# Performance work log

Hardware: AMD Instinct MI355X
Metric: run time of the kernel (lower is better)

## Reference

```python
import jax, jax.numpy as jnp
import numpy as np

B, T, H = 1024, 256, 128

def _gru(x, Wx, Wh, b):
    # Keras GRU (reset_after=True), gate order z, r, h. x: [B,T,D], b: [2,3H]
    xp = x @ Wx + b[0]                      # [B,T,3H]
    h0 = jnp.zeros((x.shape[0], Wh.shape[0]), x.dtype)
    def step(h, xt):
        hp = h @ Wh + b[1]
        xz, xr, xh = jnp.split(xt, 3, axis=-1)
        hz, hr, hn = jnp.split(hp, 3, axis=-1)
        z = jax.nn.sigmoid(xz + hz)
        r = jax.nn.sigmoid(xr + hr)
        hh = jnp.tanh(xh + r * hn)
        return z * h + (1.0 - z) * hh, None
    h, _ = jax.lax.scan(step, h0, jnp.swapaxes(xp, 0, 1))
    return h                                 # [B,H]

def setup_inputs() -> dict:
    key = jax.random.key(0)
    ks = jax.random.split(key, 32)
    def gp(k, shape, scale=0.05):
        return (jax.random.normal(k, shape, dtype=jnp.float32) * scale)
    inp = {
        "spatial": jax.random.normal(ks[0], (B, T, 2), dtype=jnp.float32),
        "hour_idx": jax.random.randint(ks[1], (B, T), 0, 24, dtype=jnp.int32),
        "week_idx": jax.random.randint(ks[2], (B, T), 0, 7, dtype=jnp.int32),
        "E_time": gp(ks[3], (24, H)),
        "E_week": gp(ks[4], (7, H)),
        # spatial GRU (input dim 2)
        "Ws_x": gp(ks[5], (2, 3 * H)), "Ws_h": gp(ks[6], (H, 3 * H)), "bs": gp(ks[7], (2, 3 * H)),
        # hour temporal GRU (input dim 128)
        "Wh_x": gp(ks[8], (H, 3 * H)), "Wh_h": gp(ks[9], (H, 3 * H)), "bh": gp(ks[10], (2, 3 * H)),
        # week temporal GRU (input dim 128)
        "Ww_x": gp(ks[11], (H, 3 * H)), "Ww_h": gp(ks[12], (H, 3 * H)), "bw": gp(ks[13], (2, 3 * H)),
        # attention Dense(3) over the channel axis of size 3
        "Wa": gp(ks[14], (3, 3)), "ba": gp(ks[15], (3,)),
        # MLP
        "W1": gp(ks[16], (H, 1024)), "b1": gp(ks[17], (1024,)),
        "W2": gp(ks[18], (1024, 512)), "b2": gp(ks[19], (512,)),
        "W3": gp(ks[20], (512, 256)), "b3": gp(ks[21], (256,)),
        "W4": gp(ks[22], (256, H)), "b4": gp(ks[23], (H,)),
        "Wo": gp(ks[24], (H, 1)), "bo": gp(ks[25], (1,)),
    }
    return inp

def reference(spatial, hour_idx, week_idx, E_time, E_week,
              Ws_x, Ws_h, bs, Wh_x, Wh_h, bh, Ww_x, Ww_h, bw,
              Wa, ba, W1, b1, W2, b2, W3, b3, W4, b4, Wo, bo):
    te = E_time[hour_idx]                    # [B,T,128] gather
    we = E_week[week_idx]                    # [B,T,128] gather
    fs = _gru(spatial, Ws_x, Ws_h, bs)       # [B,128]
    fh = _gru(te, Wh_x, Wh_h, bh)            # [B,128]
    fw = _gru(we, Ww_x, Ww_h, bw)            # [B,128]
    allf = jnp.stack([fs, fh, fw], axis=-1)  # [B,128,3]
    scores = jax.nn.softmax(jax.nn.relu(allf @ Wa + ba), axis=-1)
    sf = jnp.sum(allf * scores, axis=-1)     # [B,128] attention-fused features
    x = jax.nn.relu(sf @ W1 + b1)
    x = jax.nn.relu(x @ W2 + b2)
    x = jax.nn.relu(x @ W3 + b3)
    x = jax.nn.relu(x @ W4 + b4)
    out = (x + sf) @ Wo + bo                 # residual then Dense(1)
    return out[:, 0]                         # [B]
```

## Files before the change

### kernel.cpp

```cpp
#include <hip/hip_runtime.h>
#include <hip/hip_bf16.h>

typedef __attribute__((ext_vector_type(8))) short short8;
typedef __attribute__((ext_vector_type(4))) float f32x4;
typedef __attribute__((ext_vector_type(2))) float f32x2;

#define LOG2E  1.44269504088896340736f
#define NLOG2E (-1.44269504088896340736f)
#define TLOG2E (2.88539008177792681472f)

#define HES 168

__device__ __forceinline__ unsigned short f2bf(float f) {
  unsigned u = __builtin_bit_cast(unsigned, f);
  u += 0x7fffu + ((u >> 16) & 1u);
  return (unsigned short)(u >> 16);
}

__global__ void setup_kernel(
    const float* __restrict__ E_time, const float* __restrict__ E_week,
    const float* __restrict__ Wh_x, const float* __restrict__ bh,
    const float* __restrict__ Ww_x, const float* __restrict__ bw,
    const float* __restrict__ W1, const float* __restrict__ W2,
    const float* __restrict__ W3, const float* __restrict__ W4,
    float* __restrict__ Ptime, float* __restrict__ Pweek,
    unsigned short* __restrict__ Wt)
{
  const int b = blockIdx.x;
  const int tid = threadIdx.x;
  if (b < 31) {
    const int c = tid;
    if (b < 24) {
      float acc = bh[c];
      for (int d = 0; d < 128; ++d)
        acc = fmaf(E_time[b * 128 + d], Wh_x[d * 384 + c], acc);
      Ptime[b * 384 + c] = acc;
    } else {
      const int r = b - 24;
      float acc = bw[c];
      for (int d = 0; d < 128; ++d)
        acc = fmaf(E_week[r * 128 + d], Ww_x[d * 384 + c], acc);
      Pweek[r * 384 + c] = acc;
    }
    return;
  }
  const int id = (b - 31) * 384 + tid;
  if (id >= 819200) return;
  if (id < 131072) {
    const int n = id >> 7, k = id & 127;
    Wt[id] = f2bf(W1[k * 1024 + n]);
  } else if (id < 655360) {
    const int off = id - 131072, n = off >> 10, k = off & 1023;
    Wt[id] = f2bf(W2[k * 512 + n]);
  } else if (id < 786432) {
    const int off = id - 655360, n = off >> 9, k = off & 511;
    Wt[id] = f2bf(W3[k * 256 + n]);
  } else {
    const int off = id - 786432, n = off >> 8, k = off & 255;
    Wt[id] = f2bf(W4[k * 128 + n]);
  }
}

__global__ __launch_bounds__(512, 2) void gru_kernel(
    const float* __restrict__ spatial,
    const int* __restrict__ hour_idx,
    const int* __restrict__ week_idx,
    const float* __restrict__ Ws_x,
    const float* __restrict__ Ws_h, const float* __restrict__ bs,
    const float* __restrict__ Wh_h, const float* __restrict__ bh,
    const float* __restrict__ Ww_h, const float* __restrict__ bw,
    const float* __restrict__ Ptime, const float* __restrict__ Pweek,
    float* __restrict__ fs, float* __restrict__ fh, float* __restrict__ fw)
{
  __shared__ __align__(16) unsigned short hx[2][16 * HES];

  const int tid  = threadIdx.x;
  const int lane = tid & 63;
  const int wv   = tid >> 6;
  const int ar   = lane & 15;
  const int akg  = lane >> 4;
  const int gid  = blockIdx.x;
  const int gru  = gid >> 6;
  const int row0 = (gid & 63) * 16;

  const float* __restrict__ Wh   = (gru == 0) ? Ws_h : (gru == 1) ? Wh_h : Ww_h;
  const float* __restrict__ bvec = (gru == 0) ? bs   : (gru == 1) ? bh   : bw;
  float* __restrict__ fout       = (gru == 0) ? fs   : (gru == 1) ? fh   : fw;
  const float* __restrict__ Ptab = (gru == 1) ? Ptime : Pweek;
  const int* __restrict__ idxg   = (gru == 1) ? hour_idx : week_idx;
  const int NR = (gru == 1) ? 24 : 7;

  const int j = wv * 16 + ar;

  short8 wf[15];
  #pragma unroll
  for (int g = 0; g < 2; ++g) {
    #pragma unroll
    for (int ks = 0; ks < 5; ++ks) {
      short8 f;
      #pragma unroll
      for (int q = 0; q < 8; ++q) {
        const int k = ks * 32 + akg * 8 + q;
        float v;
        if (k < 128) v = Wh[k * 384 + g * 128 + j];
        else {
          const int p = k - 128;
          if (gru == 0) v = (p == 0) ? Ws_x[g * 128 + j]
                          : (p == 1) ? Ws_x[384 + g * 128 + j] : 0.f;
          else          v = (p < NR) ? Ptab[p * 384 + g * 128 + j] : 0.f;
        }
        f[q] = (short)f2bf(v * NLOG2E);
      }
      wf[g * 5 + ks] = f;
    }
  }
  #pragma unroll
  for (int ks = 0; ks < 4; ++ks) {
    short8 f;
    #pragma unroll
    for (int q = 0; q < 8; ++q) {
      const int k = ks * 32 + akg * 8 + q;
      f[q] = (short)f2bf(Wh[k * 384 + 256 + j] * TLOG2E);
    }
    wf[10 + ks] = f;
  }
  {
    short8 f;
    #pragma unroll
    for (int q = 0; q < 8; ++q) {
      const int p = akg * 8 + q;
      float v;
      if (gru == 0) v = (p == 0) ? Ws_x[256 + j]
                      : (p == 1) ? Ws_x[384 + 256 + j] : 0.f;
      else          v = (p < NR) ? Ptab[p * 384 + 256 + j] : 0.f;
      f[q] = (short)f2bf(v * TLOG2E);
    }
    wf[14] = f;
  }

  const float bz  = (bvec[384 + j]       + (gru == 0 ? bvec[j]       : 0.f)) * NLOG2E;
  const float br  = (bvec[384 + 128 + j] + (gru == 0 ? bvec[128 + j] : 0.f)) * NLOG2E;
  const float bnh = bvec[384 + 256 + j] * TLOG2E;
  const float bnx = (gru == 0 ? bvec[256 + j] : 0.f) * TLOG2E;

  for (int e = tid; e < 2 * 16 * HES; e += 512) ((unsigned short*)hx)[e] = 0;
  __syncthreads();

  const bool mt  = (tid & 31) == 0;
  const int mrow = tid >> 5;
  int ix_prev = 0, ix_cur = 0;
  if (mt) {
    if (gru == 0) {
      const f32x2 s = *(const f32x2*)&spatial[(row0 + mrow) * 512];
      unsigned pk;
      asm("v_cvt_pk_bf16_f32 %0, %1, %2" : "=v"(pk) : "v"(s.x), "v"(s.y));
      *(unsigned*)&hx[0][mrow * HES + 128] = pk;
    } else {
      ix_cur = idxg[(row0 + mrow) * 256];
      hx[0][mrow * HES + 128 + ix_cur] = 0x3F80;
    }
  }
  __syncthreads();

  float hst[4] = {0.f, 0.f, 0.f, 0.f};

  for (int t = 0; t < 256; ++t) {
    const unsigned short* __restrict__ hb = hx[t & 1];
    unsigned short* __restrict__ ho       = hx[(t + 1) & 1];

    short8 a[5];
    #pragma unroll
    for (int ks = 0; ks < 5; ++ks)
      a[ks] = *(const short8*)&hb[ar * HES + ks * 32 + akg * 8];

    f32x2 msp = {0.f, 0.f};
    int ix_next = 0;
    const bool mact = mt && (t + 1 < 256);
    if (mact) {
      if (gru == 0) msp = *(const f32x2*)&spatial[(row0 + mrow) * 512 + 2 * (t + 1)];
      else          ix_next = idxg[(row0 + mrow) * 256 + t + 1];
    }

    f32x4 az  = {bz, bz, bz, bz};
    f32x4 arr = {br, br, br, br};
    f32x4 anh = {bnh, bnh, bnh, bnh};
    f32x4 anx = {bnx, bnx, bnx, bnx};
    #pragma unroll
    for (int ks = 0; ks < 4; ++ks) {
      az  = __builtin_amdgcn_mfma_f32_16x16x32_bf16(a[ks], wf[ks],      az,  0, 0, 0);
      arr = __builtin_amdgcn_mfma_f32_16x16x32_bf16(a[ks], wf[5 + ks],  arr, 0, 0, 0);
      anh = __builtin_amdgcn_mfma_f32_16x16x32_bf16(a[ks], wf[10 + ks], anh, 0, 0, 0);
    }
    az  = __builtin_amdgcn_mfma_f32_16x16x32_bf16(a[4], wf[4],  az,  0, 0, 0);
    arr = __builtin_amdgcn_mfma_f32_16x16x32_bf16(a[4], wf[9],  arr, 0, 0, 0);
    anx = __builtin_amdgcn_mfma_f32_16x16x32_bf16(a[4], wf[14], anx, 0, 0, 0);

    if (mact) {
      if (gru == 0) {
        unsigned pk;
        asm("v_cvt_pk_bf16_f32 %0, %1, %2" : "=v"(pk) : "v"(msp.x), "v"(msp.y));
        *(unsigned*)&ho[mrow * HES + 128] = pk;
      } else {
        if (t >= 1) ho[mrow * HES + 128 + ix_prev] = 0;
        ho[mrow * HES + 128 + ix_next] = 0x3F80;
        ix_prev = ix_cur; ix_cur = ix_next;
      }
    }

    float hn4[4];
    #pragma unroll
    for (int q = 0; q < 4; ++q) {
      const float z  = __builtin_amdgcn_rcpf(1.f + __builtin_amdgcn_exp2f(az[q]));
      const float r  = __builtin_amdgcn_rcpf(1.f + __builtin_amdgcn_exp2f(arr[q]));
      const float e  = __builtin_amdgcn_exp2f(fmaf(r, anh[q], anx[q]));
      const float hh = fmaf(-2.f, __builtin_amdgcn_rcpf(e + 1.f), 1.f);
      hn4[q] = fmaf(z, hst[q] - hh, hh);
      hst[q] = hn4[q];
    }

    #pragma unroll
    for (int q = 0; q < 4; ++q)
      ho[(akg * 4 + q) * HES + j] = f2bf(hn4[q]);

    __syncthreads();
  }

  #pragma unroll
  for (int q = 0; q < 4; ++q)
    fout[(row0 + akg * 4 + q) * 128 + j] = hst[q];
}

template<int K, int N>
__device__ __forceinline__ void mlp_layer(
    const unsigned short* __restrict__ xin, unsigned short* __restrict__ xout,
    const unsigned short* __restrict__ Wt, const float* __restrict__ bias,
    int lane, int wv, float* __restrict__ foutF)
{
  constexpr int NT = N / 64;
  const int ar  = lane & 15;
  const int akg = lane >> 4;
  f32x4 acc[NT];
  #pragma unroll
  for (int nt = 0; nt < NT; ++nt) acc[nt] = f32x4{0.f, 0.f, 0.f, 0.f};
  for (int ks = 0; ks < K / 32; ++ks) {
    const short8 a = *(const short8*)&xin[ar * 1032 + ks * 32 + akg * 8];
    #pragma unroll
    for (int nt = 0; nt < NT; ++nt) {
      const int n = wv * (N / 4) + nt * 16 + ar;
      const short8 b = *(const short8*)&Wt[n * K + ks * 32 + akg * 8];
      acc[nt] = __builtin_amdgcn_mfma_f32_16x16x32_bf16(a, b, acc[nt], 0, 0, 0);
    }
  }
  const int rbase = akg * 4;
  #pragma unroll
  for (int nt = 0; nt < NT; ++nt) {
    const int n = wv * (N / 4) + nt * 16 + ar;
    const float bv = bias[n];
    #pragma unroll
    for (int q = 0; q < 4; ++q) {
      float v = acc[nt][q] + bv;
      v = fmaxf(v, 0.f);
      xout[(rbase + q) * 1032 + n] = f2bf(v);
      if (foutF) foutF[(rbase + q) * 128 + n] = v;
    }
  }
}

__global__ __launch_bounds__(256) void attn_mlp_kernel(
    const float* __restrict__ fs, const float* __restrict__ fh, const float* __restrict__ fw,
    const float* __restrict__ Wa, const float* __restrict__ ba,
    const unsigned short* __restrict__ Wt,
    const float* __restrict__ b1, const float* __restrict__ b2,
    const float* __restrict__ b3, const float* __restrict__ b4,
    const float* __restrict__ Wo, const float* __restrict__ bo,
    float* __restrict__ out)
{
  __shared__ __align__(16) unsigned short xa[16 * 1032];
  __shared__ __align__(16) unsigned short xb[16 * 1032];
  __shared__ __align__(16) float sf_l[16 * 128];
  __shared__ __align__(16) float x4f[16 * 128];

  const int tid  = threadIdx.x;
  const int lane = tid & 63;
  const int wv   = tid >> 6;
  const int row0 = blockIdx.x * 16;

  {
    const int i  = tid >> 4;
    const int j0 = (tid & 15) * 8;
    float wa[9], bav[3];
    #pragma unroll
    for (int q = 0; q < 9; ++q) wa[q] = Wa[q];
    #pragma unroll
    for (int q = 0; q < 3; ++q) bav[q] = ba[q];
    const int base = (row0 + i) * 128 + j0;
    #pragma unroll
    for (int half = 0; half < 2; ++half) {
      const f32x4 a = *(const f32x4*)&fs[base + half * 4];
      const f32x4 b = *(const f32x4*)&fh[base + half * 4];
      const f32x4 c = *(const f32x4*)&fw[base + half * 4];
      #pragma unroll
      for (int q = 0; q < 4; ++q) {
        const float f0 = a[q], f1 = b[q], f2 = c[q];
        float s0 = f0 * wa[0] + f1 * wa[3] + f2 * wa[6] + bav[0];
        float s1 = f0 * wa[1] + f1 * wa[4] + f2 * wa[7] + bav[1];
        float s2 = f0 * wa[2] + f1 * wa[5] + f2 * wa[8] + bav[2];
        s0 = fmaxf(s0, 0.f); s1 = fmaxf(s1, 0.f); s2 = fmaxf(s2, 0.f);
        const float m  = fmaxf(s0, fmaxf(s1, s2));
        const float e0 = __builtin_amdgcn_exp2f((s0 - m) * LOG2E);
        const float e1 = __builtin_amdgcn_exp2f((s1 - m) * LOG2E);
        const float e2 = __builtin_amdgcn_exp2f((s2 - m) * LOG2E);
        const float inv = __builtin_amdgcn_rcpf(e0 + e1 + e2);
        const float sf  = (f0 * e0 + f1 * e1 + f2 * e2) * inv;
        const int jj = j0 + half * 4 + q;
        sf_l[i * 128 + jj] = sf;
        xa[i * 1032 + jj]  = f2bf(sf);
      }
    }
  }
  __syncthreads();

  mlp_layer<128, 1024>(xa, xb, Wt,          b1, lane, wv, nullptr);
  __syncthreads();
  mlp_layer<1024, 512>(xb, xa, Wt + 131072, b2, lane, wv, nullptr);
  __syncthreads();
  mlp_layer<512,  256>(xa, xb, Wt + 655360, b3, lane, wv, nullptr);
  __syncthreads();
  mlp_layer<256,  128>(xb, xa, Wt + 786432, b4, lane, wv, x4f);
  __syncthreads();

  const int row = tid >> 4;
  const int p   = tid & 15;
  float part = 0.f;
  #pragma unroll
  for (int q = 0; q < 8; ++q) {
    const int jj = p + q * 16;
    part += (x4f[row * 128 + jj] + sf_l[row * 128 + jj]) * Wo[jj];
  }
  #pragma unroll
  for (int off = 8; off > 0; off >>= 1)
    part += __shfl_xor(part, off, 16);
  if (p == 0) out[row0 + row] = part + bo[0];
}

extern "C" void kernel_launch(void* const* d_in, const int* in_sizes, int n_in,
                              void* d_out, int out_size, void* d_ws, size_t ws_size,
                              hipStream_t stream) {
  const float* spatial  = (const float*)d_in[0];
  const int*   hour_idx = (const int*)d_in[1];
  const int*   week_idx = (const int*)d_in[2];
  const float* E_time   = (const float*)d_in[3];
  const float* E_week   = (const float*)d_in[4];
  const float* Ws_x = (const float*)d_in[5];
  const float* Ws_h = (const float*)d_in[6];
  const float* bs   = (const float*)d_in[7];
  const float* Wh_x = (const float*)d_in[8];
  const float* Wh_h = (const float*)d_in[9];
  const float* bh   = (const float*)d_in[10];
  const float* Ww_x = (const float*)d_in[11];
  const float* Ww_h = (const float*)d_in[12];
  const float* bw   = (const float*)d_in[13];
  const float* Wa   = (const float*)d_in[14];
  const float* ba   = (const float*)d_in[15];
  const float* W1   = (const float*)d_in[16];
  const float* b1   = (const float*)d_in[17];
  const float* W2   = (const float*)d_in[18];
  const float* b2   = (const float*)d_in[19];
  const float* W3   = (const float*)d_in[20];
  const float* b3   = (const float*)d_in[21];
  const float* W4   = (const float*)d_in[22];
  const float* b4   = (const float*)d_in[23];
  const float* Wo   = (const float*)d_in[24];
  const float* bo   = (const float*)d_in[25];
  float* out = (float*)d_out;

  float* ws    = (float*)d_ws;
  float* Ptime = ws;
  float* Pweek = Ptime + 9216;
  float* fsb   = Pweek + 2688;
  float* fhb   = fsb + 131072;
  float* fwb   = fhb + 131072;
  unsigned short* Wt = (unsigned short*)(fwb + 131072);

  setup_kernel<<<31 + 2134, 384, 0, stream>>>(E_time, E_week, Wh_x, bh, Ww_x, bw,
      W1, W2, W3, W4, Ptime, Pweek, Wt);
  gru_kernel<<<192, 512, 0, stream>>>(spatial, hour_idx, week_idx, Ws_x,
      Ws_h, bs, Wh_h, bh, Ww_h, bw, Ptime, Pweek, fsb, fhb, fwb);
  attn_mlp_kernel<<<64, 256, 0, stream>>>(fsb, fhb, fwb, Wa, ba, Wt,
      b1, b2, b3, b4, Wo, bo, out);
}
```

Measured before the change: 240.7 us.

## Stagger GRU row halves to overlap gate math with MFMAs; tile weight transpose

The GRU recurrence now uses a single hidden-state buffer and splits each wave's rows into two groups advancing half a step apart. While one group's gate nonlinearities and state writes run, the MFMAs for the other group's next step are issued, aiming to hide the latency of the serial gate chain. The cost is twice as many MFMA passes and barriers per timestep, since each pass computes all 16 rows but only half are consumed. Separately, the bf16 weight transpose in the setup kernel now goes through a 64x64 shared-memory tile, so both the global reads and the global writes are coalesced.

```diff
diff --git a/kernel.cpp b/kernel.cpp
--- a/kernel.cpp
+++ b/kernel.cpp
@@ -17,7 +17,7 @@
   return (unsigned short)(u >> 16);
 }
 
-__global__ void setup_kernel(
+__global__ __launch_bounds__(256) void setup_kernel(
     const float* __restrict__ E_time, const float* __restrict__ E_week,
     const float* __restrict__ Wh_x, const float* __restrict__ bh,
     const float* __restrict__ Ww_x, const float* __restrict__ bw,
@@ -29,36 +29,38 @@
   const int b = blockIdx.x;
   const int tid = threadIdx.x;
   if (b < 31) {
-    const int c = tid;
-    if (b < 24) {
-      float acc = bh[c];
-      for (int d = 0; d < 128; ++d)
-        acc = fmaf(E_time[b * 128 + d], Wh_x[d * 384 + c], acc);
-      Ptime[b * 384 + c] = acc;
-    } else {
-      const int r = b - 24;
-      float acc = bw[c];
-      for (int d = 0; d < 128; ++d)
-        acc = fmaf(E_week[r * 128 + d], Ww_x[d * 384 + c], acc);
-      Pweek[r * 384 + c] = acc;
+    for (int c = tid; c < 384; c += 256) {
+      if (b < 24) {
+        float acc = bh[c];
+        for (int d = 0; d < 128; ++d)
+          acc = fmaf(E_time[b * 128 + d], Wh_x[d * 384 + c], acc);
+        Ptime[b * 384 + c] = acc;
+      } else {
+        const int r = b - 24;
+        float acc = bw[c];
+        for (int d = 0; d < 128; ++d)
+          acc = fmaf(E_week[r * 128 + d], Ww_x[d * 384 + c], acc);
+        Pweek[r * 384 + c] = acc;
+      }
     }
     return;
   }
-  const int id = (b - 31) * 384 + tid;
-  if (id >= 819200) return;
-  if (id < 131072) {
-    const int n = id >> 7, k = id & 127;
-    Wt[id] = f2bf(W1[k * 1024 + n]);
-  } else if (id < 655360) {
-    const int off = id - 131072, n = off >> 10, k = off & 1023;
-    Wt[id] = f2bf(W2[k * 512 + n]);
-  } else if (id < 786432) {
-    const int off = id - 655360, n = off >> 9, k = off & 511;
-    Wt[id] = f2bf(W3[k * 256 + n]);
-  } else {
-    const int off = id - 786432, n = off >> 8, k = off & 255;
-    Wt[id] = f2bf(W4[k * 128 + n]);
-  }
+  __shared__ float tile[64][65];
+  int tb = b - 31;
+  const float* src; unsigned short* dst; int K, N, tk, tn;
+  if (tb < 32)       { src = W1; dst = Wt;          K = 128;  N = 1024; tk = tb >> 4; tn = tb & 15; }
+  else if (tb < 160) { tb -= 32;  src = W2; dst = Wt + 131072; K = 1024; N = 512;  tk = tb >> 3; tn = tb & 7; }
+  else if (tb < 192) { tb -= 160; src = W3; dst = Wt + 655360; K = 512;  N = 256;  tk = tb >> 2; tn = tb & 3; }
+  else               { tb -= 192; src = W4; dst = Wt + 786432; K = 256;  N = 128;  tk = tb >> 1; tn = tb & 1; }
+  const int tx = tid & 63, ty = tid >> 6;
+  const int k0 = tk * 64, n0 = tn * 64;
+  #pragma unroll
+  for (int i = 0; i < 16; ++i)
+    tile[ty * 16 + i][tx] = src[(k0 + ty * 16 + i) * N + n0 + tx];
+  __syncthreads();
+  #pragma unroll
+  for (int i = 0; i < 16; ++i)
+    dst[(n0 + ty * 16 + i) * K + k0 + tx] = f2bf(tile[tx][ty * 16 + i]);
 }
 
 __global__ __launch_bounds__(512, 2) void gru_kernel(
@@ -72,7 +74,7 @@
     const float* __restrict__ Ptime, const float* __restrict__ Pweek,
     float* __restrict__ fs, float* __restrict__ fh, float* __restrict__ fw)
 {
-  __shared__ __align__(16) unsigned short hx[2][16 * HES];
+  __shared__ __align__(16) unsigned short hx[16 * HES];
 
   const int tid  = threadIdx.x;
   const int lane = tid & 63;
@@ -143,91 +145,111 @@
   const float bnh = bvec[384 + 256 + j] * TLOG2E;
   const float bnx = (gru == 0 ? bvec[256 + j] : 0.f) * TLOG2E;
 
-  for (int e = tid; e < 2 * 16 * HES; e += 512) ((unsigned short*)hx)[e] = 0;
-  __syncthreads();
-
-  const bool mt  = (tid & 31) == 0;
-  const int mrow = tid >> 5;
-  int ix_prev = 0, ix_cur = 0;
+  for (int e = tid; e < 16 * HES; e += 512) hx[e] = 0;
+  __syncthreads();
+
+  const bool mt   = (tid & 31) == 0;
+  const int mrow  = tid >> 5;
+  const int mgrp  = (mrow >> 1) & 1;
+  f32x2 spn = {0.f, 0.f};
+  int ixc = 0, ixn = 0;
   if (mt) {
     if (gru == 0) {
-      const f32x2 s = *(const f32x2*)&spatial[(row0 + mrow) * 512];
+      const f32x2 s0 = *(const f32x2*)&spatial[(row0 + mrow) * 512];
       unsigned pk;
-      asm("v_cvt_pk_bf16_f32 %0, %1, %2" : "=v"(pk) : "v"(s.x), "v"(s.y));
-      *(unsigned*)&hx[0][mrow * HES + 128] = pk;
+      asm("v_cvt_pk_bf16_f32 %0, %1, %2" : "=v"(pk) : "v"(s0.x), "v"(s0.y));
+      *(unsigned*)&hx[mrow * HES + 128] = pk;
+      spn = *(const f32x2*)&spatial[(row0 + mrow) * 512 + 2];
     } else {
-      ix_cur = idxg[(row0 + mrow) * 256];
-      hx[0][mrow * HES + 128 + ix_cur] = 0x3F80;
+      ixc = idxg[(row0 + mrow) * 256];
+      hx[mrow * HES + 128 + ixc] = 0x3F80;
+      ixn = idxg[(row0 + mrow) * 256 + 1];
     }
   }
   __syncthreads();
 
   float hst[4] = {0.f, 0.f, 0.f, 0.f};
-
-  for (int t = 0; t < 256; ++t) {
-    const unsigned short* __restrict__ hb = hx[t & 1];
-    unsigned short* __restrict__ ho       = hx[(t + 1) & 1];
-
-    short8 a[5];
-    #pragma unroll
-    for (int ks = 0; ks < 5; ++ks)
-      a[ks] = *(const short8*)&hb[ar * HES + ks * 32 + akg * 8];
-
-    f32x2 msp = {0.f, 0.f};
-    int ix_next = 0;
-    const bool mact = mt && (t + 1 < 256);
-    if (mact) {
-      if (gru == 0) msp = *(const f32x2*)&spatial[(row0 + mrow) * 512 + 2 * (t + 1)];
-      else          ix_next = idxg[(row0 + mrow) * 256 + t + 1];
-    }
-
-    f32x4 az  = {bz, bz, bz, bz};
-    f32x4 arr = {br, br, br, br};
-    f32x4 anh = {bnh, bnh, bnh, bnh};
-    f32x4 anx = {bnx, bnx, bnx, bnx};
-    #pragma unroll
-    for (int ks = 0; ks < 4; ++ks) {
-      az  = __builtin_amdgcn_mfma_f32_16x16x32_bf16(a[ks], wf[ks],      az,  0, 0, 0);
-      arr = __builtin_amdgcn_mfma_f32_16x16x32_bf16(a[ks], wf[5 + ks],  arr, 0, 0, 0);
-      anh = __builtin_amdgcn_mfma_f32_16x16x32_bf16(a[ks], wf[10 + ks], anh, 0, 0, 0);
-    }
-    az  = __builtin_amdgcn_mfma_f32_16x16x32_bf16(a[4], wf[4],  az,  0, 0, 0);
-    arr = __builtin_amdgcn_mfma_f32_16x16x32_bf16(a[4], wf[9],  arr, 0, 0, 0);
-    anx = __builtin_amdgcn_mfma_f32_16x16x32_bf16(a[4], wf[14], anx, 0, 0, 0);
-
-    if (mact) {
-      if (gru == 0) {
-        unsigned pk;
-        asm("v_cvt_pk_bf16_f32 %0, %1, %2" : "=v"(pk) : "v"(msp.x), "v"(msp.y));
-        *(unsigned*)&ho[mrow * HES + 128] = pk;
-      } else {
-        if (t >= 1) ho[mrow * HES + 128 + ix_prev] = 0;
-        ho[mrow * HES + 128 + ix_next] = 0x3F80;
-        ix_prev = ix_cur; ix_cur = ix_next;
-      }
-    }
-
-    float hn4[4];
-    #pragma unroll
-    for (int q = 0; q < 4; ++q) {
-      const float z  = __builtin_amdgcn_rcpf(1.f + __builtin_amdgcn_exp2f(az[q]));
-      const float r  = __builtin_amdgcn_rcpf(1.f + __builtin_amdgcn_exp2f(arr[q]));
-      const float e  = __builtin_amdgcn_exp2f(fmaf(r, anh[q], anx[q]));
-      const float hh = fmaf(-2.f, __builtin_amdgcn_rcpf(e + 1.f), 1.f);
-      hn4[q] = fmaf(z, hst[q] - hh, hh);
-      hst[q] = hn4[q];
-    }
-
-    #pragma unroll
-    for (int q = 0; q < 4; ++q)
-      ho[(akg * 4 + q) * HES + j] = f2bf(hn4[q]);
-
+  const int abase = ar * HES;
+
+#define DSREAD(AV) { _Pragma("unroll") \
+  for (int ks = 0; ks < 5; ++ks) \
+    AV[ks] = *(const short8*)&hx[abase + ks * 32 + akg * 8]; }
+
+#define MFMA_ALL(AV, AZ, AR_, ANH, ANX) { \
+  AZ  = (f32x4){bz, bz, bz, bz}; \
+  AR_ = (f32x4){br, br, br, br}; \
+  ANH = (f32x4){bnh, bnh, bnh, bnh}; \
+  ANX = (f32x4){bnx, bnx, bnx, bnx}; \
+  _Pragma("unroll") for (int ks = 0; ks < 4; ++ks) { \
+    AZ  = __builtin_amdgcn_mfma_f32_16x16x32_bf16(AV[ks], wf[ks],      AZ,  0, 0, 0); \
+    AR_ = __builtin_amdgcn_mfma_f32_16x16x32_bf16(AV[ks], wf[5 + ks],  AR_, 0, 0, 0); \
+    ANH = __builtin_amdgcn_mfma_f32_16x16x32_bf16(AV[ks], wf[10 + ks], ANH, 0, 0, 0); } \
+  AZ  = __builtin_amdgcn_mfma_f32_16x16x32_bf16(AV[4], wf[4],  AZ,  0, 0, 0); \
+  AR_ = __builtin_amdgcn_mfma_f32_16x16x32_bf16(AV[4], wf[9],  AR_, 0, 0, 0); \
+  ANX = __builtin_amdgcn_mfma_f32_16x16x32_bf16(AV[4], wf[14], ANX, 0, 0, 0); }
+
+#define GATES(Q0, AZ, AR_, ANH, ANX) { _Pragma("unroll") \
+  for (int i = 0; i < 2; ++i) { \
+    const int q = (Q0) + i; \
+    const float z  = __builtin_amdgcn_rcpf(1.f + __builtin_amdgcn_exp2f(AZ[q])); \
+    const float r  = __builtin_amdgcn_rcpf(1.f + __builtin_amdgcn_exp2f(AR_[q])); \
+    const float e  = __builtin_amdgcn_exp2f(fmaf(r, ANH[q], ANX[q])); \
+    const float hh = fmaf(-2.f, __builtin_amdgcn_rcpf(e + 1.f), 1.f); \
+    const float hn = fmaf(z, hst[q] - hh, hh); \
+    hst[q] = hn; \
+    hx[(akg * 4 + q) * HES + j] = f2bf(hn); } }
+
+#define MAINT(G, M) { \
+  if (mt && mgrp == (G) && (M) + 1 < 256) { \
+    if (gru == 0) { \
+      unsigned pk; \
+      asm("v_cvt_pk_bf16_f32 %0, %1, %2" : "=v"(pk) : "v"(spn.x), "v"(spn.y)); \
+      *(unsigned*)&hx[mrow * HES + 128] = pk; \
+      if ((M) + 2 < 256) spn = *(const f32x2*)&spatial[(row0 + mrow) * 512 + 2 * ((M) + 2)]; \
+    } else { \
+      hx[mrow * HES + 128 + ixc] = 0; \
+      hx[mrow * HES + 128 + ixn] = 0x3F80; \
+      ixc = ixn; \
+      if ((M) + 2 < 256) ixn = idxg[(row0 + mrow) * 256 + (M) + 2]; \
+    } } }
+
+  f32x4 Az, Ar_, Anh, Anx, Bz, Br_, Bnh, Bnx;
+  {
+    short8 a0[5];
+    DSREAD(a0);
+    MFMA_ALL(a0, Az, Ar_, Anh, Anx);
     __syncthreads();
+  }
+
+  for (int m = 0; m < 256; ++m) {
+    {
+      short8 a1[5];
+      DSREAD(a1);
+      GATES(0, Az, Ar_, Anh, Anx);
+      MAINT(0, m);
+      MFMA_ALL(a1, Bz, Br_, Bnh, Bnx);
+      __syncthreads();
+    }
+    if (m < 255) {
+      short8 a2[5];
+      DSREAD(a2);
+      GATES(2, Bz, Br_, Bnh, Bnx);
+      MAINT(1, m);
+      MFMA_ALL(a2, Az, Ar_, Anh, Anx);
+      __syncthreads();
+    } else {
+      GATES(2, Bz, Br_, Bnh, Bnx);
+    }
   }
 
   #pragma unroll
   for (int q = 0; q < 4; ++q)
     fout[(row0 + akg * 4 + q) * 128 + j] = hst[q];
+
+#undef DSREAD
+#undef MFMA_ALL
+#undef GATES
+#undef MAINT
 }
 
 template<int K, int N>
@@ -382,7 +404,7 @@
   float* fwb   = fhb + 131072;
   unsigned short* Wt = (unsigned short*)(fwb + 131072);
 
-  setup_kernel<<<31 + 2134, 384, 0, stream>>>(E_time, E_week, Wh_x, bh, Ww_x, bw,
+  setup_kernel<<<231, 256, 0, stream>>>(E_time, E_week, Wh_x, bh, Ww_x, bw,
       W1, W2, W3, W4, Ptime, Pweek, Wt);
   gru_kernel<<<192, 512, 0, stream>>>(spatial, hour_idx, week_idx, Ws_x,
       Ws_h, bs, Wh_h, bh, Ww_h, bw, Ptime, Pweek, fsb, fhb, fwb);
```

Measured after the change: 305.3 us. 1.27x slower.

## Halve GRU block width, fold MLP weight transpose into spare GRU blocks

Applied to the files above, without the earlier changes.

GRU blocks now use 4 waves of 256 threads, each wave computing two 16-column halves, instead of 8 waves covering one half each. This doubles MFMA work per wave but halves the threads taking part in each per-step barrier. The MLP weight transpose to bf16 moves out of the setup kernel into 64 extra blocks of the GRU launch, using a shared-memory tiled transpose so it runs alongside the recurrence. Sigmoid and tanh reciprocals are paired to share one rcp per two values, and the spatial and index inputs are prefetched one step further ahead. The trade-off is less wave parallelism per step and higher register pressure from two weight fragment sets.

```diff
diff --git a/kernel.cpp b/kernel.cpp
--- a/kernel.cpp
+++ b/kernel.cpp
@@ -17,19 +17,14 @@
   return (unsigned short)(u >> 16);
 }
 
-__global__ void setup_kernel(
+__global__ __launch_bounds__(256) void ptab_kernel(
     const float* __restrict__ E_time, const float* __restrict__ E_week,
     const float* __restrict__ Wh_x, const float* __restrict__ bh,
     const float* __restrict__ Ww_x, const float* __restrict__ bw,
-    const float* __restrict__ W1, const float* __restrict__ W2,
-    const float* __restrict__ W3, const float* __restrict__ W4,
-    float* __restrict__ Ptime, float* __restrict__ Pweek,
-    unsigned short* __restrict__ Wt)
+    float* __restrict__ Ptime, float* __restrict__ Pweek)
 {
   const int b = blockIdx.x;
-  const int tid = threadIdx.x;
-  if (b < 31) {
-    const int c = tid;
+  for (int c = threadIdx.x; c < 384; c += 256) {
     if (b < 24) {
       float acc = bh[c];
       for (int d = 0; d < 128; ++d)
@@ -42,26 +37,10 @@
         acc = fmaf(E_week[r * 128 + d], Ww_x[d * 384 + c], acc);
       Pweek[r * 384 + c] = acc;
     }
-    return;
-  }
-  const int id = (b - 31) * 384 + tid;
-  if (id >= 819200) return;
-  if (id < 131072) {
-    const int n = id >> 7, k = id & 127;
-    Wt[id] = f2bf(W1[k * 1024 + n]);
-  } else if (id < 655360) {
-    const int off = id - 131072, n = off >> 10, k = off & 1023;
-    Wt[id] = f2bf(W2[k * 512 + n]);
-  } else if (id < 786432) {
-    const int off = id - 655360, n = off >> 9, k = off & 511;
-    Wt[id] = f2bf(W3[k * 256 + n]);
-  } else {
-    const int off = id - 786432, n = off >> 8, k = off & 255;
-    Wt[id] = f2bf(W4[k * 128 + n]);
-  }
-}
-
-__global__ __launch_bounds__(512, 2) void gru_kernel(
+  }
+}
+
+__global__ __launch_bounds__(256, 1) void gru_kernel(
     const float* __restrict__ spatial,
     const int* __restrict__ hour_idx,
     const int* __restrict__ week_idx,
@@ -70,11 +49,37 @@
     const float* __restrict__ Wh_h, const float* __restrict__ bh,
     const float* __restrict__ Ww_h, const float* __restrict__ bw,
     const float* __restrict__ Ptime, const float* __restrict__ Pweek,
+    const float* __restrict__ W1, const float* __restrict__ W2,
+    const float* __restrict__ W3, const float* __restrict__ W4,
+    unsigned short* __restrict__ Wt,
     float* __restrict__ fs, float* __restrict__ fh, float* __restrict__ fw)
 {
   __shared__ __align__(16) unsigned short hx[2][16 * HES];
-
-  const int tid  = threadIdx.x;
+  __shared__ float ttile[64][65];
+
+  const int tid = threadIdx.x;
+
+  if (blockIdx.x >= 192) {
+    const int tx = tid & 63, ty = tid >> 6;
+    for (int t = blockIdx.x - 192; t < 200; t += 64) {
+      const float* src; unsigned short* dst; int K, N, tk, tn; int tb = t;
+      if (tb < 32)       { src = W1; dst = Wt;          K = 128;  N = 1024; tk = tb >> 4; tn = tb & 15; }
+      else if (tb < 160) { tb -= 32;  src = W2; dst = Wt + 131072; K = 1024; N = 512;  tk = tb >> 3; tn = tb & 7; }
+      else if (tb < 192) { tb -= 160; src = W3; dst = Wt + 655360; K = 512;  N = 256;  tk = tb >> 2; tn = tb & 3; }
+      else               { tb -= 192; src = W4; dst = Wt + 786432; K = 256;  N = 128;  tk = tb >> 1; tn = tb & 1; }
+      const int k0 = tk * 64, n0 = tn * 64;
+      #pragma unroll
+      for (int i = 0; i < 16; ++i)
+        ttile[ty * 16 + i][tx] = src[(k0 + ty * 16 + i) * N + n0 + tx];
+      __syncthreads();
+      #pragma unroll
+      for (int i = 0; i < 16; ++i)
+        dst[(n0 + ty * 16 + i) * K + k0 + tx] = f2bf(ttile[tx][ty * 16 + i]);
+      __syncthreads();
+    }
+    return;
+  }
+
   const int lane = tid & 63;
   const int wv   = tid >> 6;
   const int ar   = lane & 15;
@@ -90,79 +95,96 @@
   const int* __restrict__ idxg   = (gru == 1) ? hour_idx : week_idx;
   const int NR = (gru == 1) ? 24 : 7;
 
-  const int j = wv * 16 + ar;
-
-  short8 wf[15];
-  #pragma unroll
-  for (int g = 0; g < 2; ++g) {
-    #pragma unroll
-    for (int ks = 0; ks < 5; ++ks) {
+  const int jc[2] = {wv * 16 + ar, 64 + wv * 16 + ar};
+
+  short8 wf[2][15];
+  #pragma unroll
+  for (int jh = 0; jh < 2; ++jh) {
+    #pragma unroll
+    for (int g = 0; g < 2; ++g) {
+      #pragma unroll
+      for (int ks = 0; ks < 5; ++ks) {
+        short8 f;
+        #pragma unroll
+        for (int q = 0; q < 8; ++q) {
+          const int k = ks * 32 + akg * 8 + q;
+          const int col = g * 128 + jc[jh];
+          float v;
+          if (k < 128) v = Wh[k * 384 + col];
+          else {
+            const int p = k - 128;
+            if (gru == 0) v = (p == 0) ? Ws_x[col] : (p == 1) ? Ws_x[384 + col] : 0.f;
+            else          v = (p < NR) ? Ptab[p * 384 + col] : 0.f;
+          }
+          f[q] = (short)f2bf(v * NLOG2E);
+        }
+        wf[jh][g * 5 + ks] = f;
+      }
+    }
+    #pragma unroll
+    for (int ks = 0; ks < 4; ++ks) {
       short8 f;
       #pragma unroll
       for (int q = 0; q < 8; ++q) {
         const int k = ks * 32 + akg * 8 + q;
+        f[q] = (short)f2bf(Wh[k * 384 + 256 + jc[jh]] * TLOG2E);
+      }
+      wf[jh][10 + ks] = f;
+    }
+    {
+      short8 f;
+      #pragma unroll
+      for (int q = 0; q < 8; ++q) {
+        const int p = akg * 8 + q;
+        const int col = 256 + jc[jh];
         float v;
-        if (k < 128) v = Wh[k * 384 + g * 128 + j];
-        else {
-          const int p = k - 128;
-          if (gru == 0) v = (p == 0) ? Ws_x[g * 128 + j]
-                          : (p == 1) ? Ws_x[384 + g * 128 + j] : 0.f;
-          else          v = (p < NR) ? Ptab[p * 384 + g * 128 + j] : 0.f;
-        }
-        f[q] = (short)f2bf(v * NLOG2E);
-      }
-      wf[g * 5 + ks] = f;
-    }
-  }
-  #pragma unroll
-  for (int ks = 0; ks < 4; ++ks) {
-    short8 f;
-    #pragma unroll
-    for (int q = 0; q < 8; ++q) {
-      const int k = ks * 32 + akg * 8 + q;
-      f[q] = (short)f2bf(Wh[k * 384 + 256 + j] * TLOG2E);
-    }
-    wf[10 + ks] = f;
-  }
-  {
-    short8 f;
-    #pragma unroll
-    for (int q = 0; q < 8; ++q) {
-      const int p = akg * 8 + q;
-      float v;
-      if (gru == 0) v = (p == 0) ? Ws_x[256 + j]
-                      : (p == 1) ? Ws_x[384 + 256 + j] : 0.f;
-      else          v = (p < NR) ? Ptab[p * 384 + 256 + j] : 0.f;
-      f[q] = (short)f2bf(v * TLOG2E);
-    }
-    wf[14] = f;
-  }
-
-  const float bz  = (bvec[384 + j]       + (gru == 0 ? bvec[j]       : 0.f)) * NLOG2E;
-  const float br  = (bvec[384 + 128 + j] + (gru == 0 ? bvec[128 + j] : 0.f)) * NLOG2E;
-  const float bnh = bvec[384 + 256 + j] * TLOG2E;
-  const float bnx = (gru == 0 ? bvec[256 + j] : 0.f) * TLOG2E;
-
-  for (int e = tid; e < 2 * 16 * HES; e += 512) ((unsigned short*)hx)[e] = 0;
-  __syncthreads();
-
-  const bool mt  = (tid & 31) == 0;
-  const int mrow = tid >> 5;
-  int ix_prev = 0, ix_cur = 0;
+        if (gru == 0) v = (p == 0) ? Ws_x[col] : (p == 1) ? Ws_x[384 + col] : 0.f;
+        else          v = (p < NR) ? Ptab[p * 384 + col] : 0.f;
+        f[q] = (short)f2bf(v * TLOG2E);
+      }
+      wf[jh][14] = f;
+    }
+  }
+
+  float bz[2], br[2], bnh[2], bnx[2];
+  #pragma unroll
+  for (int jh = 0; jh < 2; ++jh) {
+    const int j = jc[jh];
+    bz[jh]  = (bvec[384 + j]       + (gru == 0 ? bvec[j]       : 0.f)) * NLOG2E;
+    br[jh]  = (bvec[384 + 128 + j] + (gru == 0 ? bvec[128 + j] : 0.f)) * NLOG2E;
+    bnh[jh] = bvec[384 + 256 + j] * TLOG2E;
+    bnx[jh] = (gru == 0 ? bvec[256 + j] : 0.f) * TLOG2E;
+  }
+
+  for (int e = tid; e < 2 * 16 * HES; e += 256) ((unsigned short*)hx)[e] = 0;
+  __syncthreads();
+
+  const bool mt  = (tid & 15) == 0;
+  const int mrow = tid >> 4;
+  f32x2 spn = {0.f, 0.f};
+  int ix_prev = 0, ix_cur = 0, ix_next = 0;
   if (mt) {
     if (gru == 0) {
-      const f32x2 s = *(const f32x2*)&spatial[(row0 + mrow) * 512];
+      const f32x2 s0 = *(const f32x2*)&spatial[(row0 + mrow) * 512];
       unsigned pk;
-      asm("v_cvt_pk_bf16_f32 %0, %1, %2" : "=v"(pk) : "v"(s.x), "v"(s.y));
+      asm("v_cvt_pk_bf16_f32 %0, %1, %2" : "=v"(pk) : "v"(s0.x), "v"(s0.y));
       *(unsigned*)&hx[0][mrow * HES + 128] = pk;
+      spn = *(const f32x2*)&spatial[(row0 + mrow) * 512 + 2];
     } else {
       ix_cur = idxg[(row0 + mrow) * 256];
       hx[0][mrow * HES + 128 + ix_cur] = 0x3F80;
-    }
-  }
-  __syncthreads();
-
-  float hst[4] = {0.f, 0.f, 0.f, 0.f};
+      ix_next = idxg[(row0 + mrow) * 256 + 1];
+    }
+  }
+  __syncthreads();
+
+  float hst[2][4];
+  #pragma unroll
+  for (int jh = 0; jh < 2; ++jh)
+    #pragma unroll
+    for (int q = 0; q < 4; ++q) hst[jh][q] = 0.f;
+
+  const int abase = ar * HES;
 
   for (int t = 0; t < 256; ++t) {
     const unsigned short* __restrict__ hb = hx[t & 1];
@@ -171,63 +193,95 @@
     short8 a[5];
     #pragma unroll
     for (int ks = 0; ks < 5; ++ks)
-      a[ks] = *(const short8*)&hb[ar * HES + ks * 32 + akg * 8];
+      a[ks] = *(const short8*)&hb[abase + ks * 32 + akg * 8];
 
     f32x2 msp = {0.f, 0.f};
-    int ix_next = 0;
+    int ixn2 = 0;
     const bool mact = mt && (t + 1 < 256);
-    if (mact) {
-      if (gru == 0) msp = *(const f32x2*)&spatial[(row0 + mrow) * 512 + 2 * (t + 1)];
-      else          ix_next = idxg[(row0 + mrow) * 256 + t + 1];
-    }
-
-    f32x4 az  = {bz, bz, bz, bz};
-    f32x4 arr = {br, br, br, br};
-    f32x4 anh = {bnh, bnh, bnh, bnh};
-    f32x4 anx = {bnx, bnx, bnx, bnx};
-    #pragma unroll
-    for (int ks = 0; ks < 4; ++ks) {
-      az  = __builtin_amdgcn_mfma_f32_16x16x32_bf16(a[ks], wf[ks],      az,  0, 0, 0);
-      arr = __builtin_amdgcn_mfma_f32_16x16x32_bf16(a[ks], wf[5 + ks],  arr, 0, 0, 0);
-      anh = __builtin_amdgcn_mfma_f32_16x16x32_bf16(a[ks], wf[10 + ks], anh, 0, 0, 0);
-    }
-    az  = __builtin_amdgcn_mfma_f32_16x16x32_bf16(a[4], wf[4],  az,  0, 0, 0);
-    arr = __builtin_amdgcn_mfma_f32_16x16x32_bf16(a[4], wf[9],  arr, 0, 0, 0);
-    anx = __builtin_amdgcn_mfma_f32_16x16x32_bf16(a[4], wf[14], anx, 0, 0, 0);
+    if (mact && gru == 0 && t + 2 < 256)
+      msp = *(const f32x2*)&spatial[(row0 + mrow) * 512 + 2 * (t + 2)];
+    if (mact && gru != 0 && t + 2 < 256)
+      ixn2 = idxg[(row0 + mrow) * 256 + t + 2];
+
+    #pragma unroll
+    for (int jh = 0; jh < 2; ++jh) {
+      f32x4 az  = {bz[jh],  bz[jh],  bz[jh],  bz[jh]};
+      f32x4 arr = {br[jh],  br[jh],  br[jh],  br[jh]};
+      f32x4 anh = {bnh[jh], bnh[jh], bnh[jh], bnh[jh]};
+      f32x4 anx = {bnx[jh], bnx[jh], bnx[jh], bnx[jh]};
+      #pragma unroll
+      for (int ks = 0; ks < 4; ++ks) {
+        az  = __builtin_amdgcn_mfma_f32_16x16x32_bf16(a[ks], wf[jh][ks],      az,  0, 0, 0);
+        arr = __builtin_amdgcn_mfma_f32_16x16x32_bf16(a[ks], wf[jh][5 + ks],  arr, 0, 0, 0);
+        anh = __builtin_amdgcn_mfma_f32_16x16x32_bf16(a[ks], wf[jh][10 + ks], anh, 0, 0, 0);
+      }
+      az  = __builtin_amdgcn_mfma_f32_16x16x32_bf16(a[4], wf[jh][4],  az,  0, 0, 0);
+      arr = __builtin_amdgcn_mfma_f32_16x16x32_bf16(a[4], wf[jh][9],  arr, 0, 0, 0);
+      anx = __builtin_amdgcn_mfma_f32_16x16x32_bf16(a[4], wf[jh][14], anx, 0, 0, 0);
+
+      float zg[4], rg[4], pz[4], pr[4];
+      #pragma unroll
+      for (int q = 0; q < 4; ++q) {
+        pz[q] = 1.f + __builtin_amdgcn_exp2f(az[q]);
+        pr[q] = 1.f + __builtin_amdgcn_exp2f(arr[q]);
+      }
+      #pragma unroll
+      for (int p = 0; p < 4; p += 2) {
+        const float A0 = pz[p] * pr[p];
+        const float A1 = pz[p + 1] * pr[p + 1];
+        const float inv = __builtin_amdgcn_rcpf(A0 * A1);
+        const float t1 = A1 * inv, t0 = A0 * inv;
+        zg[p]     = pr[p] * t1;     rg[p]     = pz[p] * t1;
+        zg[p + 1] = pr[p + 1] * t0; rg[p + 1] = pz[p + 1] * t0;
+      }
+      float ph[4];
+      #pragma unroll
+      for (int q = 0; q < 4; ++q)
+        ph[q] = 1.f + __builtin_amdgcn_exp2f(fmaf(rg[q], anh[q], anx[q]));
+      float hn4[4];
+      #pragma unroll
+      for (int p = 0; p < 4; p += 2) {
+        const float inv = __builtin_amdgcn_rcpf(ph[p] * ph[p + 1]);
+        const float i0 = ph[p + 1] * inv;
+        const float i1 = ph[p] * inv;
+        const float hh0 = fmaf(-2.f, i0, 1.f);
+        const float hh1 = fmaf(-2.f, i1, 1.f);
+        hn4[p]     = fmaf(zg[p],     hst[jh][p]     - hh0, hh0);
+        hn4[p + 1] = fmaf(zg[p + 1], hst[jh][p + 1] - hh1, hh1);
+        hst[jh][p] = hn4[p]; hst[jh][p + 1] = hn4[p + 1];
+      }
+
+      unsigned p01, p23;
+      asm("v_cvt_pk_bf16_f32 %0, %1, %2" : "=v"(p01) : "v"(hn4[0]), "v"(hn4[1]));
+      asm("v_cvt_pk_bf16_f32 %0, %1, %2" : "=v"(p23) : "v"(hn4[2]), "v"(hn4[3]));
+      const int j = jc[jh];
+      ho[(akg * 4 + 0) * HES + j] = (unsigned short)(p01 & 0xffffu);
+      ho[(akg * 4 + 1) * HES + j] = (unsigned short)(p01 >> 16);
+      ho[(akg * 4 + 2) * HES + j] = (unsigned short)(p23 & 0xffffu);
+      ho[(akg * 4 + 3) * HES + j] = (unsigned short)(p23 >> 16);
+    }
 
     if (mact) {
       if (gru == 0) {
         unsigned pk;
-        asm("v_cvt_pk_bf16_f32 %0, %1, %2" : "=v"(pk) : "v"(msp.x), "v"(msp.y));
+        asm("v_cvt_pk_bf16_f32 %0, %1, %2" : "=v"(pk) : "v"(spn.x), "v"(spn.y));
         *(unsigned*)&ho[mrow * HES + 128] = pk;
+        spn = msp;
       } else {
         if (t >= 1) ho[mrow * HES + 128 + ix_prev] = 0;
         ho[mrow * HES + 128 + ix_next] = 0x3F80;
-        ix_prev = ix_cur; ix_cur = ix_next;
-      }
-    }
-
-    float hn4[4];
-    #pragma unroll
-    for (int q = 0; q < 4; ++q) {
-      const float z  = __builtin_amdgcn_rcpf(1.f + __builtin_amdgcn_exp2f(az[q]));
-      const float r  = __builtin_amdgcn_rcpf(1.f + __builtin_amdgcn_exp2f(arr[q]));
-      const float e  = __builtin_amdgcn_exp2f(fmaf(r, anh[q], anx[q]));
-      const float hh = fmaf(-2.f, __builtin_amdgcn_rcpf(e + 1.f), 1.f);
-      hn4[q] = fmaf(z, hst[q] - hh, hh);
-      hst[q] = hn4[q];
-    }
-
+        ix_prev = ix_cur; ix_cur = ix_next; ix_next = ixn2;
+      }
+    }
+
+    __syncthreads();
+  }
+
+  #pragma unroll
+  for (int jh = 0; jh < 2; ++jh)
     #pragma unroll
     for (int q = 0; q < 4; ++q)
-      ho[(akg * 4 + q) * HES + j] = f2bf(hn4[q]);
-
-    __syncthreads();
-  }
-
-  #pragma unroll
-  for (int q = 0; q < 4; ++q)
-    fout[(row0 + akg * 4 + q) * 128 + j] = hst[q];
+      fout[(row0 + akg * 4 + q) * 128 + jc[jh]] = hst[jh][q];
 }
 
 template<int K, int N>
@@ -382,10 +436,10 @@
   float* fwb   = fhb + 131072;
   unsigned short* Wt = (unsigned short*)(fwb + 131072);
 
-  setup_kernel<<<31 + 2134, 384, 0, stream>>>(E_time, E_week, Wh_x, bh, Ww_x, bw,
-      W1, W2, W3, W4, Ptime, Pweek, Wt);
-  gru_kernel<<<192, 512, 0, stream>>>(spatial, hour_idx, week_idx, Ws_x,
-      Ws_h, bs, Wh_h, bh, Ww_h, bw, Ptime, Pweek, fsb, fhb, fwb);
+  ptab_kernel<<<31, 256, 0, stream>>>(E_time, E_week, Wh_x, bh, Ww_x, bw, Ptime, Pweek);
+  gru_kernel<<<256, 256, 0, stream>>>(spatial, hour_idx, week_idx, Ws_x,
+      Ws_h, bs, Wh_h, bh, Ww_h, bw, Ptime, Pweek,
+      W1, W2, W3, W4, Wt, fsb, fhb, fwb);
   attn_mlp_kernel<<<64, 256, 0, stream>>>(fsb, fhb, fwb, Wa, ba, Wt,
       b1, b2, b3, b4, Wo, bo, out);
 }
```

After: 280.2 us. +16.4%, slower.
